# Optimization experiments

Hardware: AMD Instinct MI355X
Metric: run time of the kernel (lower is better)

The kernel has to match this reference:

```python
import jax, jax.numpy as jnp
import numpy as np
from math import sqrt

N_HEADS = 4
IN_FEATURES = 64
KQ = 64
HEAD_V = IN_FEATURES // N_HEADS  # 16


def setup_inputs() -> dict:
    key = jax.random.key(0)
    ks = jax.random.split(key, 7)
    s = 0.05
    x = jax.random.normal(ks[0], (8192, IN_FEATURES), dtype=jnp.float32)
    # Per-head Linear weights stacked on a leading head axis.
    # torch Linear: y = x @ W.T + b; we store W already transposed: [H, F, E]
    Wq = jax.random.normal(ks[1], (N_HEADS, IN_FEATURES, KQ), dtype=jnp.float32) * s
    bq = jax.random.normal(ks[2], (N_HEADS, KQ), dtype=jnp.float32) * s
    Wk = jax.random.normal(ks[3], (N_HEADS, IN_FEATURES, KQ), dtype=jnp.float32) * s
    bk = jax.random.normal(ks[4], (N_HEADS, KQ), dtype=jnp.float32) * s
    Wv = jax.random.normal(ks[5], (N_HEADS, IN_FEATURES, HEAD_V), dtype=jnp.float32) * s
    bv = jax.random.normal(ks[6], (N_HEADS, HEAD_V), dtype=jnp.float32) * s
    return {"x": x, "Wq": Wq, "bq": bq, "Wk": Wk, "bk": bk, "Wv": Wv, "bv": bv}


def reference(x, Wq, bq, Wk, bk, Wv, bv):
    N, F = x.shape
    scale = 1.0 / sqrt(F)  # original divides by sqrt(in_features), NOT sqrt(kq)
    # Batched-head projections: [H, N, E]
    Q = jnp.einsum('nf,hfe->hne', x, Wq) + bq[:, None, :]
    K = jnp.einsum('nf,hfe->hne', x, Wk) + bk[:, None, :]
    V = jnp.einsum('nf,hfd->hnd', x, Wv) + bv[:, None, :]
    logits = jnp.einsum('hne,hme->hnm', Q, K) * scale  # [H, N, N]
    attn = jax.nn.softmax(logits, axis=-1)
    out_heads = jnp.einsum('hnm,hmd->hnd', attn, V)    # [H, N, HEAD_V]
    # Head i writes columns [i*HEAD_V:(i+1)*HEAD_V] of the output.
    out = jnp.transpose(out_heads, (1, 0, 2)).reshape(N, F)
    return out
```

## Files before the change

### kernel.cpp

```cpp
#include <hip/hip_runtime.h>

typedef __attribute__((ext_vector_type(4))) float f32x4;
typedef __attribute__((ext_vector_type(8))) short bf16x8;
typedef __attribute__((ext_vector_type(4))) short bf16x4;
typedef long fp8x8;

#define NH 4

static __device__ __forceinline__ unsigned short f2bf(float f){
  unsigned u = __float_as_uint(f);
  u += 0x7FFFu + ((u >> 16) & 1u);
  return (unsigned short)(u >> 16);
}

static __device__ __forceinline__ unsigned pack2bf(float a, float b){
  return __builtin_amdgcn_perm(__float_as_uint(b) + 0x8000u,
                               __float_as_uint(a) + 0x8000u, 0x07060302u);
}

static __device__ __forceinline__ unsigned pack2bf_t(float a, float b){
  return __builtin_amdgcn_perm(__float_as_uint(b), __float_as_uint(a), 0x07060302u);
}

static __device__ __forceinline__ int pack_fp8x4(float a, float b, float c, float d){
  int w = __builtin_amdgcn_cvt_pk_fp8_f32(a, b, 0, false);
  w     = __builtin_amdgcn_cvt_pk_fp8_f32(c, d, w, true);
  return w;
}

__global__ __launch_bounds__(256) void wprep_kernel(
    const float* __restrict__ Wq, const float* __restrict__ bq,
    const float* __restrict__ Wk, const float* __restrict__ bk,
    const float* __restrict__ Wv,
    unsigned short* __restrict__ WF, float* __restrict__ bias_s, int n)
{
  __shared__ unsigned short wqT[64*72];
  __shared__ unsigned short wkT[64*72];
  __shared__ unsigned short wvT[16*72];

  const int t = threadIdx.x;
  const int h = blockIdx.x;
  const float S1 = 0.4246609001f;
  const int f = t >> 2, eg = t & 3;

  {
    const float4* g = (const float4*)(Wq + h*4096 + f*64 + eg*16);
    #pragma unroll
    for (int p = 0; p < 4; ++p){
      float4 d = g[p];
      int e0 = eg*16 + p*4;
      wqT[(e0+0)*72 + f] = f2bf(d.x * S1);
      wqT[(e0+1)*72 + f] = f2bf(d.y * S1);
      wqT[(e0+2)*72 + f] = f2bf(d.z * S1);
      wqT[(e0+3)*72 + f] = f2bf(d.w * S1);
    }
  }
  {
    const float4* g = (const float4*)(Wk + h*4096 + f*64 + eg*16);
    #pragma unroll
    for (int p = 0; p < 4; ++p){
      float4 d = g[p];
      int e0 = eg*16 + p*4;
      wkT[(e0+0)*72 + f] = f2bf(d.x * S1);
      wkT[(e0+1)*72 + f] = f2bf(d.y * S1);
      wkT[(e0+2)*72 + f] = f2bf(d.z * S1);
      wkT[(e0+3)*72 + f] = f2bf(d.w * S1);
    }
  }
  {
    float4 d = *(const float4*)(Wv + h*1024 + f*16 + eg*4);
    int d0 = eg*4;
    wvT[(d0+0)*72 + f] = f2bf(d.x);
    wvT[(d0+1)*72 + f] = f2bf(d.y);
    wvT[(d0+2)*72 + f] = f2bf(d.z);
    wvT[(d0+3)*72 + f] = f2bf(d.w);
  }
  if (t < 64)       bias_s[h*128 + t] = bq[h*64 + t] * S1;
  else if (t < 128) bias_s[h*128 + t] = bk[h*64 + (t-64)] * S1;
  __syncthreads();

  const int lane = t & 63, w = t >> 6;
  const int quad = lane >> 4, l16 = lane & 15;
  for (int s = w; s < 18; s += 4){
    const unsigned short* src;
    if (s < 8){      int et = s>>1,     ks = s&1;     src = wqT + (et*16+l16)*72 + ks*32 + quad*8; }
    else if (s < 16){int ft = (s-8)>>1, ks = (s-8)&1; src = wkT + (ft*16+l16)*72 + ks*32 + quad*8; }
    else {           int ks = s-16;                   src = wvT + l16*72 + ks*32 + quad*8; }
    uint4 v = *(const uint4*)src;
    *(uint4*)(WF + ((size_t)(h*18 + s)*64 + lane)*8) = v;
  }
}

__global__ __launch_bounds__(256) void proj_kernel(
    const float* __restrict__ x, const float* __restrict__ bv,
    const unsigned short* __restrict__ WF, const float* __restrict__ bias_s,
    unsigned char* __restrict__ Qfr, unsigned char* __restrict__ Kt,
    unsigned short* __restrict__ Vt, int n)
{
  __shared__ unsigned short xf[8*64*8];
  __shared__ float bql[64], bkl[64], bvl[16];

  const int t  = threadIdx.x;
  const int h  = blockIdx.y;
  const int r0 = blockIdx.x * 64;

  {
    const int r = t >> 2, cg4 = t & 3;
    const float4* g = (const float4*)(x + (size_t)(r0 + r)*64 + cg4*16);
    float4 a = g[0], b = g[1], c = g[2], d = g[3];
    unsigned u0 = pack2bf(a.x,a.y), u1 = pack2bf(a.z,a.w);
    unsigned u2 = pack2bf(b.x,b.y), u3 = pack2bf(b.z,b.w);
    unsigned u4 = pack2bf(c.x,c.y), u5 = pack2bf(c.z,c.w);
    unsigned u6 = pack2bf(d.x,d.y), u7 = pack2bf(d.z,d.w);
    const int it = r >> 4, l16r = r & 15, ks = cg4 >> 1, q0 = (cg4 & 1)*2;
    uint4* dst0 = (uint4*)(xf + ((it*2+ks)*64 + q0*16     + l16r)*8);
    uint4* dst1 = (uint4*)(xf + ((it*2+ks)*64 + (q0+1)*16 + l16r)*8);
    *dst0 = make_uint4(u0,u1,u2,u3);
    *dst1 = make_uint4(u4,u5,u6,u7);
  }
  if (t < 64)        bql[t]     = bias_s[h*128 + t];
  else if (t < 128)  bkl[t-64]  = bias_s[h*128 + t];
  else if (t < 144)  bvl[t-128] = bv[h*16 + (t-128)];
  __syncthreads();

  const int lane = t & 63, w = t >> 6;
  const int quad = lane >> 4, l16 = lane & 15;

  bf16x8 xa[8];
  #pragma unroll
  for (int i = 0; i < 8; ++i)
    xa[i] = *(const bf16x8*)(xf + (i*64 + lane)*8);

  const unsigned short* WFh = WF + (size_t)h*18*64*8;
  bf16x8 wq0 = *(const bf16x8*)(WFh + ((size_t)(     w*2 + 0)*64 + lane)*8);
  bf16x8 wq1 = *(const bf16x8*)(WFh + ((size_t)(     w*2 + 1)*64 + lane)*8);
  bf16x8 wk0 = *(const bf16x8*)(WFh + ((size_t)(8  + w*2 + 0)*64 + lane)*8);
  bf16x8 wk1 = *(const bf16x8*)(WFh + ((size_t)(8  + w*2 + 1)*64 + lane)*8);
  bf16x8 wv0 = *(const bf16x8*)(WFh + ((size_t)16*64 + lane)*8);
  bf16x8 wv1 = *(const bf16x8*)(WFh + ((size_t)17*64 + lane)*8);

  const f32x4 z = {0.f,0.f,0.f,0.f};
  f32x4 accQ[4] = {z,z,z,z};
  f32x4 accK[4] = {z,z,z,z};
  f32x4 accV = z;

  #pragma unroll
  for (int it = 0; it < 4; ++it){
    accQ[it] = __builtin_amdgcn_mfma_f32_16x16x32_bf16(wq0, xa[it*2+0], accQ[it], 0,0,0);
    accQ[it] = __builtin_amdgcn_mfma_f32_16x16x32_bf16(wq1, xa[it*2+1], accQ[it], 0,0,0);
  }
  #pragma unroll
  for (int tt = 0; tt < 4; ++tt){
    accK[tt] = __builtin_amdgcn_mfma_f32_16x16x32_bf16(wk0, xa[tt*2+0], accK[tt], 0,0,0);
    accK[tt] = __builtin_amdgcn_mfma_f32_16x16x32_bf16(wk1, xa[tt*2+1], accK[tt], 0,0,0);
  }
  accV = __builtin_amdgcn_mfma_f32_16x16x32_bf16(xa[w*2+0], wv0, accV, 0,0,0);
  accV = __builtin_amdgcn_mfma_f32_16x16x32_bf16(xa[w*2+1], wv1, accV, 0,0,0);

  {
    const int e0 = w*16 + quad*4;
    const float b0 = bql[e0], b1 = bql[e0+1], b2 = bql[e0+2], b3 = bql[e0+3];
    const int qk = (e0 & 31) >> 3, hf = e0 >> 5, boff = (quad & 1) * 4;
    #pragma unroll
    for (int it = 0; it < 4; ++it){
      unsigned o = pack_fp8x4(accQ[it][0]+b0, accQ[it][1]+b1,
                              accQ[it][2]+b2, accQ[it][3]+b3);
      const int T = (r0 >> 4) + it;
      *(unsigned*)(Qfr + (size_t)h*((size_t)n<<6) + (size_t)T*1024
                       + (qk*16 + l16)*16 + hf*8 + boff) = o;
    }
  }
  {
    const int f0 = w*16 + quad*4;
    const float bk0 = bkl[f0], bk1 = bkl[f0+1], bk2 = bkl[f0+2], bk3 = bkl[f0+3];
    const int qk = (f0 & 31) >> 3, hf = f0 >> 5, boff = (quad & 1) * 4;
    #pragma unroll
    for (int tt = 0; tt < 4; ++tt){
      unsigned o = pack_fp8x4(accK[tt][0]+bk0, accK[tt][1]+bk1,
                              accK[tt][2]+bk2, accK[tt][3]+bk3);
      const int T = (r0 >> 4) + tt;
      *(unsigned*)(Kt + (size_t)h*((size_t)n<<6) + (size_t)T*1024
                      + (qk*16 + l16)*16 + hf*8 + boff) = o;
    }
  }
  {
    float bvv = bvl[l16];
    unsigned v01 = pack2bf(accV[0]+bvv, accV[1]+bvv);
    unsigned v23 = pack2bf(accV[2]+bvv, accV[3]+bvv);
    const int T = (r0 >> 4) + w;
    *(uint2*)(Vt + (size_t)h*((size_t)n<<4)
                 + ((size_t)(T>>1)*64 + lane)*8 + (T&1)*4) = make_uint2(v01, v23);
  }
}

__global__ __launch_bounds__(512, 4) void attn_kernel(
    const unsigned char* __restrict__ Qfr, const unsigned char* __restrict__ Kt,
    const unsigned short* __restrict__ Vt, float* __restrict__ out, int n)
{
  __shared__ float part[7][64][33];

  const int tid  = threadIdx.x;
  const int lane = tid & 63;
  const int jq   = tid >> 6;

  #pragma unroll 1
  for (int i = 0; i < jq; ++i) __builtin_amdgcn_s_sleep(3);

  const int bid  = blockIdx.x;
  const int h    = bid & 3;
  const int iblk = bid >> 2;
  const int l16  = lane & 15, quad = lane >> 4;
  const int i0   = iblk*64;
  const int ntq  = (n >> 3) >> 4;
  const int nch  = ntq >> 1;
  const int tile0 = jq * ntq;

  const unsigned char* qfh = Qfr + (size_t)h*((size_t)n<<6);
  longlong2 q0 = *(const longlong2*)(qfh + (size_t)((i0>>4)    )*1024 + lane*16);
  longlong2 q1 = *(const longlong2*)(qfh + (size_t)((i0>>4) + 1)*1024 + lane*16);
  longlong2 q2 = *(const longlong2*)(qfh + (size_t)((i0>>4) + 2)*1024 + lane*16);
  longlong2 q3 = *(const longlong2*)(qfh + (size_t)((i0>>4) + 3)*1024 + lane*16);
  const fp8x8 qf00 = (fp8x8)q0.x, qf01 = (fp8x8)q0.y;
  const fp8x8 qf10 = (fp8x8)q1.x, qf11 = (fp8x8)q1.y;
  const fp8x8 qf20 = (fp8x8)q2.x, qf21 = (fp8x8)q2.y;
  const fp8x8 qf30 = (fp8x8)q3.x, qf31 = (fp8x8)q3.y;

  const longlong2* ktl = (const longlong2*)(Kt + (size_t)h*((size_t)n<<6)) + (size_t)tile0*64 + lane;
  const uint4*     vtu = (const uint4*)(Vt + (size_t)h*((size_t)n<<4)) + (size_t)(tile0>>1)*64 + lane;

  const f32x4 z = {0.f,0.f,0.f,0.f};
  f32x4 o0 = z, o1 = z, o2 = z, o3 = z;
  f32x4 la0 = z, la1 = z, la2 = z, la3 = z;
  const bf16x8 vones = {(short)0x3F80, (short)0x3F80, (short)0x3F80, (short)0x3F80,
                        (short)0x3F80, (short)0x3F80, (short)0x3F80, (short)0x3F80};

  longlong2 ka0 = ktl[0],   ka1 = ktl[64];
  uint4     va  = vtu[0];
  longlong2 kb0 = ktl[128], kb1 = ktl[192];
  uint4     vb  = vtu[64];

#define ITILE(QA, QB, OO, LL)                                                 \
  {                                                                           \
    f32x4 s = __builtin_amdgcn_mfma_f32_16x16x32_fp8_fp8(a0, QA, z, 0,0,0);   \
    s = __builtin_amdgcn_mfma_f32_16x16x32_fp8_fp8(a1, QB, s, 0,0,0);         \
    f32x4 u = __builtin_amdgcn_mfma_f32_16x16x32_fp8_fp8(b0, QA, z, 0,0,0);   \
    u = __builtin_amdgcn_mfma_f32_16x16x32_fp8_fp8(b1, QB, u, 0,0,0);         \
    float e0 = __builtin_amdgcn_exp2f(s[0]);                                  \
    float e1 = __builtin_amdgcn_exp2f(s[1]);                                  \
    float e2 = __builtin_amdgcn_exp2f(s[2]);                                  \
    float e3 = __builtin_amdgcn_exp2f(s[3]);                                  \
    float f0 = __builtin_amdgcn_exp2f(u[0]);                                  \
    float f1 = __builtin_amdgcn_exp2f(u[1]);                                  \
    float f2 = __builtin_amdgcn_exp2f(u[2]);                                  \
    float f3 = __builtin_amdgcn_exp2f(u[3]);                                  \
    union { uint4 uu; bf16x8 v; } pq;                                         \
    pq.uu = make_uint4(pack2bf_t(e0,e1), pack2bf_t(e2,e3),                    \
                       pack2bf_t(f0,f1), pack2bf_t(f2,f3));                   \
    OO = __builtin_amdgcn_mfma_f32_16x16x32_bf16(pq.v, vfv,   OO, 0,0,0);     \
    LL = __builtin_amdgcn_mfma_f32_16x16x32_bf16(pq.v, vones, LL, 0,0,0);     \
  }

#define ATTN_CHUNK(KA, KB, VV)                                                \
  {                                                                           \
    const fp8x8 a0 = (fp8x8)KA.x, a1 = (fp8x8)KA.y;                           \
    const fp8x8 b0 = (fp8x8)KB.x, b1 = (fp8x8)KB.y;                           \
    union { uint4 uu; bf16x8 v; } vfu; vfu.uu = VV;                           \
    const bf16x8 vfv = vfu.v;                                                 \
    ITILE(qf00, qf01, o0, la0)                                                \
    ITILE(qf10, qf11, o1, la1)                                                \
    ITILE(qf20, qf21, o2, la2)                                                \
    ITILE(qf30, qf31, o3, la3)                                                \
  }

  for (int c = 0; c < nch - 2; c += 2){
    ATTN_CHUNK(ka0, ka1, va)
    ka0 = ktl[256]; ka1 = ktl[320]; va = vtu[128];
    ATTN_CHUNK(kb0, kb1, vb)
    kb0 = ktl[384]; kb1 = ktl[448]; vb = vtu[192];
    ktl += 256; vtu += 128;
    #pragma unroll
    for (int g = 0; g < 12; ++g){
      __builtin_amdgcn_sched_group_barrier(0x008, 2, 0);
      __builtin_amdgcn_sched_group_barrier(0x002, 8, 0);
    }
  }
  ATTN_CHUNK(ka0, ka1, va)
  ATTN_CHUNK(kb0, kb1, vb)
#undef ATTN_CHUNK
#undef ITILE

  if (jq > 0){
    float* p = &part[jq-1][lane][0];
    p[ 0]=o0[0];  p[ 1]=o0[1];  p[ 2]=o0[2];  p[ 3]=o0[3];
    p[ 4]=o1[0];  p[ 5]=o1[1];  p[ 6]=o1[2];  p[ 7]=o1[3];
    p[ 8]=o2[0];  p[ 9]=o2[1];  p[10]=o2[2];  p[11]=o2[3];
    p[12]=o3[0];  p[13]=o3[1];  p[14]=o3[2];  p[15]=o3[3];
    p[16]=la0[0]; p[17]=la0[1]; p[18]=la0[2]; p[19]=la0[3];
    p[20]=la1[0]; p[21]=la1[1]; p[22]=la1[2]; p[23]=la1[3];
    p[24]=la2[0]; p[25]=la2[1]; p[26]=la2[2]; p[27]=la2[3];
    p[28]=la3[0]; p[29]=la3[1]; p[30]=la3[2]; p[31]=la3[3];
  }
  __syncthreads();

  if (jq == 0){
    #pragma unroll
    for (int q = 0; q < 7; ++q){
      const float* r = &part[q][lane][0];
      o0[0] +=r[0];  o0[1] +=r[1];  o0[2] +=r[2];  o0[3] +=r[3];
      o1[0] +=r[4];  o1[1] +=r[5];  o1[2] +=r[6];  o1[3] +=r[7];
      o2[0] +=r[8];  o2[1] +=r[9];  o2[2] +=r[10]; o2[3] +=r[11];
      o3[0] +=r[12]; o3[1] +=r[13]; o3[2] +=r[14]; o3[3] +=r[15];
      la0[0]+=r[16]; la0[1]+=r[17]; la0[2]+=r[18]; la0[3]+=r[19];
      la1[0]+=r[20]; la1[1]+=r[21]; la1[2]+=r[22]; la1[3]+=r[23];
      la2[0]+=r[24]; la2[1]+=r[25]; la2[2]+=r[26]; la2[3]+=r[27];
      la3[0]+=r[28]; la3[1]+=r[29]; la3[2]+=r[30]; la3[3]+=r[31];
    }
    #pragma unroll
    for (int reg = 0; reg < 4; ++reg){
      int i = quad*4 + reg;
      out[(size_t)(i0 +      i)*64 + h*16 + l16] = o0[reg] / la0[reg];
      out[(size_t)(i0 + 16 + i)*64 + h*16 + l16] = o1[reg] / la1[reg];
      out[(size_t)(i0 + 32 + i)*64 + h*16 + l16] = o2[reg] / la2[reg];
      out[(size_t)(i0 + 48 + i)*64 + h*16 + l16] = o3[reg] / la3[reg];
    }
  }
}

extern "C" void kernel_launch(void* const* d_in, const int* in_sizes, int n_in,
                              void* d_out, int out_size, void* d_ws, size_t ws_size,
                              hipStream_t stream) {
  const float* x  = (const float*)d_in[0];
  const float* Wq = (const float*)d_in[1];
  const float* bq = (const float*)d_in[2];
  const float* Wk = (const float*)d_in[3];
  const float* bk = (const float*)d_in[4];
  const float* Wv = (const float*)d_in[5];
  const float* bv = (const float*)d_in[6];
  float* out = (float*)d_out;

  const int n = in_sizes[0] / 64;

  unsigned char* Qfr  = (unsigned char*)d_ws;
  unsigned char* Kt   = Qfr + (size_t)NH*n*64;
  unsigned short* Vt  = (unsigned short*)(Kt + (size_t)NH*n*64);
  unsigned short* WF  = Vt + (size_t)NH*n*16;
  float* bias_s       = (float*)(WF + (size_t)NH*18*64*8);

  wprep_kernel<<<NH, 256, 0, stream>>>(Wq, bq, Wk, bk, Wv, WF, bias_s, n);
  proj_kernel<<<dim3(n/64, NH), 256, 0, stream>>>(x, bv, WF, bias_s, Qfr, Kt, Vt, n);
  attn_kernel<<<dim3((n/64)*NH), 512, 0, stream>>>(Qfr, Kt, Vt, out, n);
}
```

Measured before the change: 118.5 us.

## Fuse weight prep, projection and attention into one cooperative kernel

Merges the three launches (weight prep, QKV projection, attention) into a single cooperative kernel with a grid-wide sync between the projection and attention phases. Each block now redoes the weight transpose/convert in LDS (aliased onto the partial-sum buffer) instead of reading a prepared global copy. It also retunes the attention loop's scheduling group barriers. The three-kernel path is kept as a fallback if the cooperative launch fails. The aim is to remove launch gaps and tail effects, at the cost of a grid barrier, redundant per-block weight prep, and a requirement that all 512 blocks be co-resident.

```diff
diff --git a/kernel.cpp b/kernel.cpp
--- a/kernel.cpp
+++ b/kernel.cpp
@@ -1,8 +1,10 @@
 #include <hip/hip_runtime.h>
+#include <hip/hip_cooperative_groups.h>
+
+namespace cg = cooperative_groups;
 
 typedef __attribute__((ext_vector_type(4))) float f32x4;
 typedef __attribute__((ext_vector_type(8))) short bf16x8;
-typedef __attribute__((ext_vector_type(4))) short bf16x4;
 typedef long fp8x8;
 
 #define NH 4
@@ -27,217 +29,6 @@
   w     = __builtin_amdgcn_cvt_pk_fp8_f32(c, d, w, true);
   return w;
 }
-
-__global__ __launch_bounds__(256) void wprep_kernel(
-    const float* __restrict__ Wq, const float* __restrict__ bq,
-    const float* __restrict__ Wk, const float* __restrict__ bk,
-    const float* __restrict__ Wv,
-    unsigned short* __restrict__ WF, float* __restrict__ bias_s, int n)
-{
-  __shared__ unsigned short wqT[64*72];
-  __shared__ unsigned short wkT[64*72];
-  __shared__ unsigned short wvT[16*72];
-
-  const int t = threadIdx.x;
-  const int h = blockIdx.x;
-  const float S1 = 0.4246609001f;
-  const int f = t >> 2, eg = t & 3;
-
-  {
-    const float4* g = (const float4*)(Wq + h*4096 + f*64 + eg*16);
-    #pragma unroll
-    for (int p = 0; p < 4; ++p){
-      float4 d = g[p];
-      int e0 = eg*16 + p*4;
-      wqT[(e0+0)*72 + f] = f2bf(d.x * S1);
-      wqT[(e0+1)*72 + f] = f2bf(d.y * S1);
-      wqT[(e0+2)*72 + f] = f2bf(d.z * S1);
-      wqT[(e0+3)*72 + f] = f2bf(d.w * S1);
-    }
-  }
-  {
-    const float4* g = (const float4*)(Wk + h*4096 + f*64 + eg*16);
-    #pragma unroll
-    for (int p = 0; p < 4; ++p){
-      float4 d = g[p];
-      int e0 = eg*16 + p*4;
-      wkT[(e0+0)*72 + f] = f2bf(d.x * S1);
-      wkT[(e0+1)*72 + f] = f2bf(d.y * S1);
-      wkT[(e0+2)*72 + f] = f2bf(d.z * S1);
-      wkT[(e0+3)*72 + f] = f2bf(d.w * S1);
-    }
-  }
-  {
-    float4 d = *(const float4*)(Wv + h*1024 + f*16 + eg*4);
-    int d0 = eg*4;
-    wvT[(d0+0)*72 + f] = f2bf(d.x);
-    wvT[(d0+1)*72 + f] = f2bf(d.y);
-    wvT[(d0+2)*72 + f] = f2bf(d.z);
-    wvT[(d0+3)*72 + f] = f2bf(d.w);
-  }
-  if (t < 64)       bias_s[h*128 + t] = bq[h*64 + t] * S1;
-  else if (t < 128) bias_s[h*128 + t] = bk[h*64 + (t-64)] * S1;
-  __syncthreads();
-
-  const int lane = t & 63, w = t >> 6;
-  const int quad = lane >> 4, l16 = lane & 15;
-  for (int s = w; s < 18; s += 4){
-    const unsigned short* src;
-    if (s < 8){      int et = s>>1,     ks = s&1;     src = wqT + (et*16+l16)*72 + ks*32 + quad*8; }
-    else if (s < 16){int ft = (s-8)>>1, ks = (s-8)&1; src = wkT + (ft*16+l16)*72 + ks*32 + quad*8; }
-    else {           int ks = s-16;                   src = wvT + l16*72 + ks*32 + quad*8; }
-    uint4 v = *(const uint4*)src;
-    *(uint4*)(WF + ((size_t)(h*18 + s)*64 + lane)*8) = v;
-  }
-}
-
-__global__ __launch_bounds__(256) void proj_kernel(
-    const float* __restrict__ x, const float* __restrict__ bv,
-    const unsigned short* __restrict__ WF, const float* __restrict__ bias_s,
-    unsigned char* __restrict__ Qfr, unsigned char* __restrict__ Kt,
-    unsigned short* __restrict__ Vt, int n)
-{
-  __shared__ unsigned short xf[8*64*8];
-  __shared__ float bql[64], bkl[64], bvl[16];
-
-  const int t  = threadIdx.x;
-  const int h  = blockIdx.y;
-  const int r0 = blockIdx.x * 64;
-
-  {
-    const int r = t >> 2, cg4 = t & 3;
-    const float4* g = (const float4*)(x + (size_t)(r0 + r)*64 + cg4*16);
-    float4 a = g[0], b = g[1], c = g[2], d = g[3];
-    unsigned u0 = pack2bf(a.x,a.y), u1 = pack2bf(a.z,a.w);
-    unsigned u2 = pack2bf(b.x,b.y), u3 = pack2bf(b.z,b.w);
-    unsigned u4 = pack2bf(c.x,c.y), u5 = pack2bf(c.z,c.w);
-    unsigned u6 = pack2bf(d.x,d.y), u7 = pack2bf(d.z,d.w);
-    const int it = r >> 4, l16r = r & 15, ks = cg4 >> 1, q0 = (cg4 & 1)*2;
-    uint4* dst0 = (uint4*)(xf + ((it*2+ks)*64 + q0*16     + l16r)*8);
-    uint4* dst1 = (uint4*)(xf + ((it*2+ks)*64 + (q0+1)*16 + l16r)*8);
-    *dst0 = make_uint4(u0,u1,u2,u3);
-    *dst1 = make_uint4(u4,u5,u6,u7);
-  }
-  if (t < 64)        bql[t]     = bias_s[h*128 + t];
-  else if (t < 128)  bkl[t-64]  = bias_s[h*128 + t];
-  else if (t < 144)  bvl[t-128] = bv[h*16 + (t-128)];
-  __syncthreads();
-
-  const int lane = t & 63, w = t >> 6;
-  const int quad = lane >> 4, l16 = lane & 15;
-
-  bf16x8 xa[8];
-  #pragma unroll
-  for (int i = 0; i < 8; ++i)
-    xa[i] = *(const bf16x8*)(xf + (i*64 + lane)*8);
-
-  const unsigned short* WFh = WF + (size_t)h*18*64*8;
-  bf16x8 wq0 = *(const bf16x8*)(WFh + ((size_t)(     w*2 + 0)*64 + lane)*8);
-  bf16x8 wq1 = *(const bf16x8*)(WFh + ((size_t)(     w*2 + 1)*64 + lane)*8);
-  bf16x8 wk0 = *(const bf16x8*)(WFh + ((size_t)(8  + w*2 + 0)*64 + lane)*8);
-  bf16x8 wk1 = *(const bf16x8*)(WFh + ((size_t)(8  + w*2 + 1)*64 + lane)*8);
-  bf16x8 wv0 = *(const bf16x8*)(WFh + ((size_t)16*64 + lane)*8);
-  bf16x8 wv1 = *(const bf16x8*)(WFh + ((size_t)17*64 + lane)*8);
-
-  const f32x4 z = {0.f,0.f,0.f,0.f};
-  f32x4 accQ[4] = {z,z,z,z};
-  f32x4 accK[4] = {z,z,z,z};
-  f32x4 accV = z;
-
-  #pragma unroll
-  for (int it = 0; it < 4; ++it){
-    accQ[it] = __builtin_amdgcn_mfma_f32_16x16x32_bf16(wq0, xa[it*2+0], accQ[it], 0,0,0);
-    accQ[it] = __builtin_amdgcn_mfma_f32_16x16x32_bf16(wq1, xa[it*2+1], accQ[it], 0,0,0);
-  }
-  #pragma unroll
-  for (int tt = 0; tt < 4; ++tt){
-    accK[tt] = __builtin_amdgcn_mfma_f32_16x16x32_bf16(wk0, xa[tt*2+0], accK[tt], 0,0,0);
-    accK[tt] = __builtin_amdgcn_mfma_f32_16x16x32_bf16(wk1, xa[tt*2+1], accK[tt], 0,0,0);
-  }
-  accV = __builtin_amdgcn_mfma_f32_16x16x32_bf16(xa[w*2+0], wv0, accV, 0,0,0);
-  accV = __builtin_amdgcn_mfma_f32_16x16x32_bf16(xa[w*2+1], wv1, accV, 0,0,0);
-
-  {
-    const int e0 = w*16 + quad*4;
-    const float b0 = bql[e0], b1 = bql[e0+1], b2 = bql[e0+2], b3 = bql[e0+3];
-    const int qk = (e0 & 31) >> 3, hf = e0 >> 5, boff = (quad & 1) * 4;
-    #pragma unroll
-    for (int it = 0; it < 4; ++it){
-      unsigned o = pack_fp8x4(accQ[it][0]+b0, accQ[it][1]+b1,
-                              accQ[it][2]+b2, accQ[it][3]+b3);
-      const int T = (r0 >> 4) + it;
-      *(unsigned*)(Qfr + (size_t)h*((size_t)n<<6) + (size_t)T*1024
-                       + (qk*16 + l16)*16 + hf*8 + boff) = o;
-    }
-  }
-  {
-    const int f0 = w*16 + quad*4;
-    const float bk0 = bkl[f0], bk1 = bkl[f0+1], bk2 = bkl[f0+2], bk3 = bkl[f0+3];
-    const int qk = (f0 & 31) >> 3, hf = f0 >> 5, boff = (quad & 1) * 4;
-    #pragma unroll
-    for (int tt = 0; tt < 4; ++tt){
-      unsigned o = pack_fp8x4(accK[tt][0]+bk0, accK[tt][1]+bk1,
-                              accK[tt][2]+bk2, accK[tt][3]+bk3);
-      const int T = (r0 >> 4) + tt;
-      *(unsigned*)(Kt + (size_t)h*((size_t)n<<6) + (size_t)T*1024
-                      + (qk*16 + l16)*16 + hf*8 + boff) = o;
-    }
-  }
-  {
-    float bvv = bvl[l16];
-    unsigned v01 = pack2bf(accV[0]+bvv, accV[1]+bvv);
-    unsigned v23 = pack2bf(accV[2]+bvv, accV[3]+bvv);
-    const int T = (r0 >> 4) + w;
-    *(uint2*)(Vt + (size_t)h*((size_t)n<<4)
-                 + ((size_t)(T>>1)*64 + lane)*8 + (T&1)*4) = make_uint2(v01, v23);
-  }
-}
-
-__global__ __launch_bounds__(512, 4) void attn_kernel(
-    const unsigned char* __restrict__ Qfr, const unsigned char* __restrict__ Kt,
-    const unsigned short* __restrict__ Vt, float* __restrict__ out, int n)
-{
-  __shared__ float part[7][64][33];
-
-  const int tid  = threadIdx.x;
-  const int lane = tid & 63;
-  const int jq   = tid >> 6;
-
-  #pragma unroll 1
-  for (int i = 0; i < jq; ++i) __builtin_amdgcn_s_sleep(3);
-
-  const int bid  = blockIdx.x;
-  const int h    = bid & 3;
-  const int iblk = bid >> 2;
-  const int l16  = lane & 15, quad = lane >> 4;
-  const int i0   = iblk*64;
-  const int ntq  = (n >> 3) >> 4;
-  const int nch  = ntq >> 1;
-  const int tile0 = jq * ntq;
-
-  const unsigned char* qfh = Qfr + (size_t)h*((size_t)n<<6);
-  longlong2 q0 = *(const longlong2*)(qfh + (size_t)((i0>>4)    )*1024 + lane*16);
-  longlong2 q1 = *(const longlong2*)(qfh + (size_t)((i0>>4) + 1)*1024 + lane*16);
-  longlong2 q2 = *(const longlong2*)(qfh + (size_t)((i0>>4) + 2)*1024 + lane*16);
-  longlong2 q3 = *(const longlong2*)(qfh + (size_t)((i0>>4) + 3)*1024 + lane*16);
-  const fp8x8 qf00 = (fp8x8)q0.x, qf01 = (fp8x8)q0.y;
-  const fp8x8 qf10 = (fp8x8)q1.x, qf11 = (fp8x8)q1.y;
-  const fp8x8 qf20 = (fp8x8)q2.x, qf21 = (fp8x8)q2.y;
-  const fp8x8 qf30 = (fp8x8)q3.x, qf31 = (fp8x8)q3.y;
-
-  const longlong2* ktl = (const longlong2*)(Kt + (size_t)h*((size_t)n<<6)) + (size_t)tile0*64 + lane;
-  const uint4*     vtu = (const uint4*)(Vt + (size_t)h*((size_t)n<<4)) + (size_t)(tile0>>1)*64 + lane;
-
-  const f32x4 z = {0.f,0.f,0.f,0.f};
-  f32x4 o0 = z, o1 = z, o2 = z, o3 = z;
-  f32x4 la0 = z, la1 = z, la2 = z, la3 = z;
-  const bf16x8 vones = {(short)0x3F80, (short)0x3F80, (short)0x3F80, (short)0x3F80,
-                        (short)0x3F80, (short)0x3F80, (short)0x3F80, (short)0x3F80};
-
-  longlong2 ka0 = ktl[0],   ka1 = ktl[64];
-  uint4     va  = vtu[0];
-  longlong2 kb0 = ktl[128], kb1 = ktl[192];
-  uint4     vb  = vtu[64];
 
 #define ITILE(QA, QB, OO, LL)                                                 \
   {                                                                           \
@@ -272,22 +63,468 @@
     ITILE(qf30, qf31, o3, la3)                                                \
   }
 
+#define ATTN_SGB                                                              \
+    _Pragma("unroll")                                                         \
+    for (int g = 0; g < 16; ++g){                                             \
+      __builtin_amdgcn_sched_group_barrier(0x008, 3, 0);                      \
+      __builtin_amdgcn_sched_group_barrier(0x002, 6, 0);                      \
+    }
+
+__global__ __launch_bounds__(512, 4) void fused_kernel(
+    const float* __restrict__ x,
+    const float* __restrict__ Wq, const float* __restrict__ bq,
+    const float* __restrict__ Wk, const float* __restrict__ bk,
+    const float* __restrict__ Wv, const float* __restrict__ bv,
+    unsigned char* __restrict__ Qfr, unsigned char* __restrict__ Kt,
+    unsigned short* __restrict__ Vt, float* __restrict__ out, int n)
+{
+  __shared__ float part[7][64][33];
+  __shared__ float bql[64], bkl[64], bvl[16];
+
+  unsigned short* wqT = (unsigned short*)&part[0][0][0];
+  unsigned short* wkT = wqT + 64*72;
+  unsigned short* wvT = wkT + 64*72;
+  unsigned short* xf  = (unsigned short*)&part[0][0][0];
+
+  const int t    = threadIdx.x;
+  const int lane = t & 63;
+  const int w    = t >> 6;
+  const int bid  = blockIdx.x;
+  const int h    = bid & 3;
+  const int iblk = bid >> 2;
+  const int r0   = iblk * 64;
+  const int quad = lane >> 4, l16 = lane & 15;
+  const float S1 = 0.4246609001f;
+  const f32x4 z  = {0.f,0.f,0.f,0.f};
+
+  if (t < 256){
+    const int f = t >> 2, eg = t & 3;
+    {
+      const float4* g = (const float4*)(Wq + h*4096 + f*64 + eg*16);
+      #pragma unroll
+      for (int p = 0; p < 4; ++p){
+        float4 d = g[p]; int e0 = eg*16 + p*4;
+        wqT[(e0+0)*72 + f] = f2bf(d.x * S1);
+        wqT[(e0+1)*72 + f] = f2bf(d.y * S1);
+        wqT[(e0+2)*72 + f] = f2bf(d.z * S1);
+        wqT[(e0+3)*72 + f] = f2bf(d.w * S1);
+      }
+    }
+    {
+      const float4* g = (const float4*)(Wk + h*4096 + f*64 + eg*16);
+      #pragma unroll
+      for (int p = 0; p < 4; ++p){
+        float4 d = g[p]; int e0 = eg*16 + p*4;
+        wkT[(e0+0)*72 + f] = f2bf(d.x * S1);
+        wkT[(e0+1)*72 + f] = f2bf(d.y * S1);
+        wkT[(e0+2)*72 + f] = f2bf(d.z * S1);
+        wkT[(e0+3)*72 + f] = f2bf(d.w * S1);
+      }
+    }
+    {
+      float4 d = *(const float4*)(Wv + h*1024 + f*16 + eg*4);
+      int d0 = eg*4;
+      wvT[(d0+0)*72 + f] = f2bf(d.x);
+      wvT[(d0+1)*72 + f] = f2bf(d.y);
+      wvT[(d0+2)*72 + f] = f2bf(d.z);
+      wvT[(d0+3)*72 + f] = f2bf(d.w);
+    }
+  }
+  if (t < 64)        bql[t]     = bq[h*64 + t] * S1;
+  else if (t < 128)  bkl[t-64]  = bk[h*64 + (t-64)] * S1;
+  else if (t < 144)  bvl[t-128] = bv[h*16 + (t-128)];
+  __syncthreads();
+
+  bf16x8 wq0 = {0,0,0,0,0,0,0,0}, wq1 = wq0, wk0 = wq0, wk1 = wq0,
+         wv0 = wq0, wv1 = wq0;
+  if (w < 4){
+    wq0 = *(const bf16x8*)(wqT + (w*16 + l16)*72 +      quad*8);
+    wq1 = *(const bf16x8*)(wqT + (w*16 + l16)*72 + 32 + quad*8);
+    wk0 = *(const bf16x8*)(wkT + (w*16 + l16)*72 +      quad*8);
+    wk1 = *(const bf16x8*)(wkT + (w*16 + l16)*72 + 32 + quad*8);
+    wv0 = *(const bf16x8*)(wvT + l16*72 +      quad*8);
+    wv1 = *(const bf16x8*)(wvT + l16*72 + 32 + quad*8);
+  }
+  __syncthreads();
+
+  if (t < 256){
+    const int r = t >> 2, cg4 = t & 3;
+    const float4* g = (const float4*)(x + (size_t)(r0 + r)*64 + cg4*16);
+    float4 a = g[0], b = g[1], c = g[2], d = g[3];
+    unsigned u0 = pack2bf(a.x,a.y), u1 = pack2bf(a.z,a.w);
+    unsigned u2 = pack2bf(b.x,b.y), u3 = pack2bf(b.z,b.w);
+    unsigned u4 = pack2bf(c.x,c.y), u5 = pack2bf(c.z,c.w);
+    unsigned u6 = pack2bf(d.x,d.y), u7 = pack2bf(d.z,d.w);
+    const int it = r >> 4, l16r = r & 15, ks = cg4 >> 1, q0 = (cg4 & 1)*2;
+    uint4* dst0 = (uint4*)(xf + ((it*2+ks)*64 + q0*16     + l16r)*8);
+    uint4* dst1 = (uint4*)(xf + ((it*2+ks)*64 + (q0+1)*16 + l16r)*8);
+    *dst0 = make_uint4(u0,u1,u2,u3);
+    *dst1 = make_uint4(u4,u5,u6,u7);
+  }
+  __syncthreads();
+
+  if (w < 4){
+    bf16x8 xa[8];
+    #pragma unroll
+    for (int i = 0; i < 8; ++i)
+      xa[i] = *(const bf16x8*)(xf + (i*64 + lane)*8);
+
+    f32x4 accQ[4] = {z,z,z,z};
+    f32x4 accK[4] = {z,z,z,z};
+    f32x4 accV = z;
+
+    #pragma unroll
+    for (int it = 0; it < 4; ++it){
+      accQ[it] = __builtin_amdgcn_mfma_f32_16x16x32_bf16(wq0, xa[it*2+0], accQ[it], 0,0,0);
+      accQ[it] = __builtin_amdgcn_mfma_f32_16x16x32_bf16(wq1, xa[it*2+1], accQ[it], 0,0,0);
+    }
+    #pragma unroll
+    for (int tt = 0; tt < 4; ++tt){
+      accK[tt] = __builtin_amdgcn_mfma_f32_16x16x32_bf16(wk0, xa[tt*2+0], accK[tt], 0,0,0);
+      accK[tt] = __builtin_amdgcn_mfma_f32_16x16x32_bf16(wk1, xa[tt*2+1], accK[tt], 0,0,0);
+    }
+    accV = __builtin_amdgcn_mfma_f32_16x16x32_bf16(xa[w*2+0], wv0, accV, 0,0,0);
+    accV = __builtin_amdgcn_mfma_f32_16x16x32_bf16(xa[w*2+1], wv1, accV, 0,0,0);
+
+    {
+      const int e0 = w*16 + quad*4;
+      const float b0 = bql[e0], b1 = bql[e0+1], b2 = bql[e0+2], b3 = bql[e0+3];
+      const int qk = (e0 & 31) >> 3, hf = e0 >> 5, boff = (quad & 1) * 4;
+      #pragma unroll
+      for (int it = 0; it < 4; ++it){
+        unsigned o = pack_fp8x4(accQ[it][0]+b0, accQ[it][1]+b1,
+                                accQ[it][2]+b2, accQ[it][3]+b3);
+        const int T = (r0 >> 4) + it;
+        *(unsigned*)(Qfr + (size_t)h*((size_t)n<<6) + (size_t)T*1024
+                         + (qk*16 + l16)*16 + hf*8 + boff) = o;
+      }
+    }
+    {
+      const int f0 = w*16 + quad*4;
+      const float bk0 = bkl[f0], bk1 = bkl[f0+1], bk2 = bkl[f0+2], bk3 = bkl[f0+3];
+      const int qk = (f0 & 31) >> 3, hf = f0 >> 5, boff = (quad & 1) * 4;
+      #pragma unroll
+      for (int tt = 0; tt < 4; ++tt){
+        unsigned o = pack_fp8x4(accK[tt][0]+bk0, accK[tt][1]+bk1,
+                                accK[tt][2]+bk2, accK[tt][3]+bk3);
+        const int T = (r0 >> 4) + tt;
+        *(unsigned*)(Kt + (size_t)h*((size_t)n<<6) + (size_t)T*1024
+                        + (qk*16 + l16)*16 + hf*8 + boff) = o;
+      }
+    }
+    {
+      float bvv = bvl[l16];
+      unsigned v01 = pack2bf(accV[0]+bvv, accV[1]+bvv);
+      unsigned v23 = pack2bf(accV[2]+bvv, accV[3]+bvv);
+      const int T = (r0 >> 4) + w;
+      *(uint2*)(Vt + (size_t)h*((size_t)n<<4)
+                   + ((size_t)(T>>1)*64 + lane)*8 + (T&1)*4) = make_uint2(v01, v23);
+    }
+  }
+
+  __threadfence();
+  cg::this_grid().sync();
+
+  const int jq = w;
+
+  #pragma unroll 1
+  for (int i = 0; i < jq; ++i) __builtin_amdgcn_s_sleep(3);
+
+  const int i0  = r0;
+  const int ntq = (n >> 3) >> 4;
+  const int nch = ntq >> 1;
+  const int tile0 = jq * ntq;
+
+  const unsigned char* qfh = Qfr + (size_t)h*((size_t)n<<6);
+  longlong2 q0 = *(const longlong2*)(qfh + (size_t)((i0>>4)    )*1024 + lane*16);
+  longlong2 q1 = *(const longlong2*)(qfh + (size_t)((i0>>4) + 1)*1024 + lane*16);
+  longlong2 q2 = *(const longlong2*)(qfh + (size_t)((i0>>4) + 2)*1024 + lane*16);
+  longlong2 q3 = *(const longlong2*)(qfh + (size_t)((i0>>4) + 3)*1024 + lane*16);
+  const fp8x8 qf00 = (fp8x8)q0.x, qf01 = (fp8x8)q0.y;
+  const fp8x8 qf10 = (fp8x8)q1.x, qf11 = (fp8x8)q1.y;
+  const fp8x8 qf20 = (fp8x8)q2.x, qf21 = (fp8x8)q2.y;
+  const fp8x8 qf30 = (fp8x8)q3.x, qf31 = (fp8x8)q3.y;
+
+  const longlong2* ktl = (const longlong2*)(Kt + (size_t)h*((size_t)n<<6)) + (size_t)tile0*64 + lane;
+  const uint4*     vtu = (const uint4*)(Vt + (size_t)h*((size_t)n<<4)) + (size_t)(tile0>>1)*64 + lane;
+
+  f32x4 o0 = z, o1 = z, o2 = z, o3 = z;
+  f32x4 la0 = z, la1 = z, la2 = z, la3 = z;
+  const bf16x8 vones = {(short)0x3F80, (short)0x3F80, (short)0x3F80, (short)0x3F80,
+                        (short)0x3F80, (short)0x3F80, (short)0x3F80, (short)0x3F80};
+
+  longlong2 ka0 = ktl[0],   ka1 = ktl[64];
+  uint4     va  = vtu[0];
+  longlong2 kb0 = ktl[128], kb1 = ktl[192];
+  uint4     vb  = vtu[64];
+
   for (int c = 0; c < nch - 2; c += 2){
     ATTN_CHUNK(ka0, ka1, va)
     ka0 = ktl[256]; ka1 = ktl[320]; va = vtu[128];
     ATTN_CHUNK(kb0, kb1, vb)
     kb0 = ktl[384]; kb1 = ktl[448]; vb = vtu[192];
     ktl += 256; vtu += 128;
-    #pragma unroll
-    for (int g = 0; g < 12; ++g){
-      __builtin_amdgcn_sched_group_barrier(0x008, 2, 0);
-      __builtin_amdgcn_sched_group_barrier(0x002, 8, 0);
-    }
+    ATTN_SGB
   }
   ATTN_CHUNK(ka0, ka1, va)
   ATTN_CHUNK(kb0, kb1, vb)
-#undef ATTN_CHUNK
-#undef ITILE
+
+  if (jq > 0){
+    float* p = &part[jq-1][lane][0];
+    p[ 0]=o0[0];  p[ 1]=o0[1];  p[ 2]=o0[2];  p[ 3]=o0[3];
+    p[ 4]=o1[0];  p[ 5]=o1[1];  p[ 6]=o1[2];  p[ 7]=o1[3];
+    p[ 8]=o2[0];  p[ 9]=o2[1];  p[10]=o2[2];  p[11]=o2[3];
+    p[12]=o3[0];  p[13]=o3[1];  p[14]=o3[2];  p[15]=o3[3];
+    p[16]=la0[0]; p[17]=la0[1]; p[18]=la0[2]; p[19]=la0[3];
+    p[20]=la1[0]; p[21]=la1[1]; p[22]=la1[2]; p[23]=la1[3];
+    p[24]=la2[0]; p[25]=la2[1]; p[26]=la2[2]; p[27]=la2[3];
+    p[28]=la3[0]; p[29]=la3[1]; p[30]=la3[2]; p[31]=la3[3];
+  }
+  __syncthreads();
+
+  if (jq == 0){
+    #pragma unroll
+    for (int q = 0; q < 7; ++q){
+      const float* r = &part[q][lane][0];
+      o0[0] +=r[0];  o0[1] +=r[1];  o0[2] +=r[2];  o0[3] +=r[3];
+      o1[0] +=r[4];  o1[1] +=r[5];  o1[2] +=r[6];  o1[3] +=r[7];
+      o2[0] +=r[8];  o2[1] +=r[9];  o2[2] +=r[10]; o2[3] +=r[11];
+      o3[0] +=r[12]; o3[1] +=r[13]; o3[2] +=r[14]; o3[3] +=r[15];
+      la0[0]+=r[16]; la0[1]+=r[17]; la0[2]+=r[18]; la0[3]+=r[19];
+      la1[0]+=r[20]; la1[1]+=r[21]; la1[2]+=r[22]; la1[3]+=r[23];
+      la2[0]+=r[24]; la2[1]+=r[25]; la2[2]+=r[26]; la2[3]+=r[27];
+      la3[0]+=r[28]; la3[1]+=r[29]; la3[2]+=r[30]; la3[3]+=r[31];
+    }
+    #pragma unroll
+    for (int reg = 0; reg < 4; ++reg){
+      int i = quad*4 + reg;
+      out[(size_t)(i0 +      i)*64 + h*16 + l16] = o0[reg] / la0[reg];
+      out[(size_t)(i0 + 16 + i)*64 + h*16 + l16] = o1[reg] / la1[reg];
+      out[(size_t)(i0 + 32 + i)*64 + h*16 + l16] = o2[reg] / la2[reg];
+      out[(size_t)(i0 + 48 + i)*64 + h*16 + l16] = o3[reg] / la3[reg];
+    }
+  }
+}
+
+__global__ __launch_bounds__(256) void wprep_kernel(
+    const float* __restrict__ Wq, const float* __restrict__ bq,
+    const float* __restrict__ Wk, const float* __restrict__ bk,
+    const float* __restrict__ Wv,
+    unsigned short* __restrict__ WF, float* __restrict__ bias_s, int n)
+{
+  __shared__ unsigned short wqT[64*72];
+  __shared__ unsigned short wkT[64*72];
+  __shared__ unsigned short wvT[16*72];
+
+  const int t = threadIdx.x;
+  const int h = blockIdx.x;
+  const float S1 = 0.4246609001f;
+  const int f = t >> 2, eg = t & 3;
+
+  {
+    const float4* g = (const float4*)(Wq + h*4096 + f*64 + eg*16);
+    #pragma unroll
+    for (int p = 0; p < 4; ++p){
+      float4 d = g[p]; int e0 = eg*16 + p*4;
+      wqT[(e0+0)*72 + f] = f2bf(d.x * S1);
+      wqT[(e0+1)*72 + f] = f2bf(d.y * S1);
+      wqT[(e0+2)*72 + f] = f2bf(d.z * S1);
+      wqT[(e0+3)*72 + f] = f2bf(d.w * S1);
+    }
+  }
+  {
+    const float4* g = (const float4*)(Wk + h*4096 + f*64 + eg*16);
+    #pragma unroll
+    for (int p = 0; p < 4; ++p){
+      float4 d = g[p]; int e0 = eg*16 + p*4;
+      wkT[(e0+0)*72 + f] = f2bf(d.x * S1);
+      wkT[(e0+1)*72 + f] = f2bf(d.y * S1);
+      wkT[(e0+2)*72 + f] = f2bf(d.z * S1);
+      wkT[(e0+3)*72 + f] = f2bf(d.w * S1);
+    }
+  }
+  {
+    float4 d = *(const float4*)(Wv + h*1024 + f*16 + eg*4);
+    int d0 = eg*4;
+    wvT[(d0+0)*72 + f] = f2bf(d.x);
+    wvT[(d0+1)*72 + f] = f2bf(d.y);
+    wvT[(d0+2)*72 + f] = f2bf(d.z);
+    wvT[(d0+3)*72 + f] = f2bf(d.w);
+  }
+  if (t < 64)       bias_s[h*128 + t] = bq[h*64 + t] * S1;
+  else if (t < 128) bias_s[h*128 + t] = bk[h*64 + (t-64)] * S1;
+  __syncthreads();
+
+  const int lane = t & 63, w = t >> 6;
+  const int quad = lane >> 4, l16 = lane & 15;
+  for (int s = w; s < 18; s += 4){
+    const unsigned short* src;
+    if (s < 8){      int et = s>>1,     ks = s&1;     src = wqT + (et*16+l16)*72 + ks*32 + quad*8; }
+    else if (s < 16){int ft = (s-8)>>1, ks = (s-8)&1; src = wkT + (ft*16+l16)*72 + ks*32 + quad*8; }
+    else {           int ks = s-16;                   src = wvT + l16*72 + ks*32 + quad*8; }
+    uint4 v = *(const uint4*)src;
+    *(uint4*)(WF + ((size_t)(h*18 + s)*64 + lane)*8) = v;
+  }
+}
+
+__global__ __launch_bounds__(256) void proj_kernel(
+    const float* __restrict__ x, const float* __restrict__ bv,
+    const unsigned short* __restrict__ WF, const float* __restrict__ bias_s,
+    unsigned char* __restrict__ Qfr, unsigned char* __restrict__ Kt,
+    unsigned short* __restrict__ Vt, int n)
+{
+  __shared__ unsigned short xf[8*64*8];
+  __shared__ float bql[64], bkl[64], bvl[16];
+
+  const int t  = threadIdx.x;
+  const int h  = blockIdx.y;
+  const int r0 = blockIdx.x * 64;
+
+  {
+    const int r = t >> 2, cg4 = t & 3;
+    const float4* g = (const float4*)(x + (size_t)(r0 + r)*64 + cg4*16);
+    float4 a = g[0], b = g[1], c = g[2], d = g[3];
+    unsigned u0 = pack2bf(a.x,a.y), u1 = pack2bf(a.z,a.w);
+    unsigned u2 = pack2bf(b.x,b.y), u3 = pack2bf(b.z,b.w);
+    unsigned u4 = pack2bf(c.x,c.y), u5 = pack2bf(c.z,c.w);
+    unsigned u6 = pack2bf(d.x,d.y), u7 = pack2bf(d.z,d.w);
+    const int it = r >> 4, l16r = r & 15, ks = cg4 >> 1, q0 = (cg4 & 1)*2;
+    uint4* dst0 = (uint4*)(xf + ((it*2+ks)*64 + q0*16     + l16r)*8);
+    uint4* dst1 = (uint4*)(xf + ((it*2+ks)*64 + (q0+1)*16 + l16r)*8);
+    *dst0 = make_uint4(u0,u1,u2,u3);
+    *dst1 = make_uint4(u4,u5,u6,u7);
+  }
+  if (t < 64)        bql[t]     = bias_s[h*128 + t];
+  else if (t < 128)  bkl[t-64]  = bias_s[h*128 + t];
+  else if (t < 144)  bvl[t-128] = bv[h*16 + (t-128)];
+  __syncthreads();
+
+  const int lane = t & 63, w = t >> 6;
+  const int quad = lane >> 4, l16 = lane & 15;
+
+  bf16x8 xa[8];
+  #pragma unroll
+  for (int i = 0; i < 8; ++i)
+    xa[i] = *(const bf16x8*)(xf + (i*64 + lane)*8);
+
+  const unsigned short* WFh = WF + (size_t)h*18*64*8;
+  bf16x8 wq0 = *(const bf16x8*)(WFh + ((size_t)(     w*2 + 0)*64 + lane)*8);
+  bf16x8 wq1 = *(const bf16x8*)(WFh + ((size_t)(     w*2 + 1)*64 + lane)*8);
+  bf16x8 wk0 = *(const bf16x8*)(WFh + ((size_t)(8  + w*2 + 0)*64 + lane)*8);
+  bf16x8 wk1 = *(const bf16x8*)(WFh + ((size_t)(8  + w*2 + 1)*64 + lane)*8);
+  bf16x8 wv0 = *(const bf16x8*)(WFh + ((size_t)16*64 + lane)*8);
+  bf16x8 wv1 = *(const bf16x8*)(WFh + ((size_t)17*64 + lane)*8);
+
+  const f32x4 z = {0.f,0.f,0.f,0.f};
+  f32x4 accQ[4] = {z,z,z,z};
+  f32x4 accK[4] = {z,z,z,z};
+  f32x4 accV = z;
+
+  #pragma unroll
+  for (int it = 0; it < 4; ++it){
+    accQ[it] = __builtin_amdgcn_mfma_f32_16x16x32_bf16(wq0, xa[it*2+0], accQ[it], 0,0,0);
+    accQ[it] = __builtin_amdgcn_mfma_f32_16x16x32_bf16(wq1, xa[it*2+1], accQ[it], 0,0,0);
+  }
+  #pragma unroll
+  for (int tt = 0; tt < 4; ++tt){
+    accK[tt] = __builtin_amdgcn_mfma_f32_16x16x32_bf16(wk0, xa[tt*2+0], accK[tt], 0,0,0);
+    accK[tt] = __builtin_amdgcn_mfma_f32_16x16x32_bf16(wk1, xa[tt*2+1], accK[tt], 0,0,0);
+  }
+  accV = __builtin_amdgcn_mfma_f32_16x16x32_bf16(xa[w*2+0], wv0, accV, 0,0,0);
+  accV = __builtin_amdgcn_mfma_f32_16x16x32_bf16(xa[w*2+1], wv1, accV, 0,0,0);
+
+  {
+    const int e0 = w*16 + quad*4;
+    const float b0 = bql[e0], b1 = bql[e0+1], b2 = bql[e0+2], b3 = bql[e0+3];
+    const int qk = (e0 & 31) >> 3, hf = e0 >> 5, boff = (quad & 1) * 4;
+    #pragma unroll
+    for (int it = 0; it < 4; ++it){
+      unsigned o = pack_fp8x4(accQ[it][0]+b0, accQ[it][1]+b1,
+                              accQ[it][2]+b2, accQ[it][3]+b3);
+      const int T = (r0 >> 4) + it;
+      *(unsigned*)(Qfr + (size_t)h*((size_t)n<<6) + (size_t)T*1024
+                       + (qk*16 + l16)*16 + hf*8 + boff) = o;
+    }
+  }
+  {
+    const int f0 = w*16 + quad*4;
+    const float bk0 = bkl[f0], bk1 = bkl[f0+1], bk2 = bkl[f0+2], bk3 = bkl[f0+3];
+    const int qk = (f0 & 31) >> 3, hf = f0 >> 5, boff = (quad & 1) * 4;
+    #pragma unroll
+    for (int tt = 0; tt < 4; ++tt){
+      unsigned o = pack_fp8x4(accK[tt][0]+bk0, accK[tt][1]+bk1,
+                              accK[tt][2]+bk2, accK[tt][3]+bk3);
+      const int T = (r0 >> 4) + tt;
+      *(unsigned*)(Kt + (size_t)h*((size_t)n<<6) + (size_t)T*1024
+                      + (qk*16 + l16)*16 + hf*8 + boff) = o;
+    }
+  }
+  {
+    float bvv = bvl[l16];
+    unsigned v01 = pack2bf(accV[0]+bvv, accV[1]+bvv);
+    unsigned v23 = pack2bf(accV[2]+bvv, accV[3]+bvv);
+    const int T = (r0 >> 4) + w;
+    *(uint2*)(Vt + (size_t)h*((size_t)n<<4)
+                 + ((size_t)(T>>1)*64 + lane)*8 + (T&1)*4) = make_uint2(v01, v23);
+  }
+}
+
+__global__ __launch_bounds__(512, 4) void attn_kernel(
+    const unsigned char* __restrict__ Qfr, const unsigned char* __restrict__ Kt,
+    const unsigned short* __restrict__ Vt, float* __restrict__ out, int n)
+{
+  __shared__ float part[7][64][33];
+
+  const int tid  = threadIdx.x;
+  const int lane = tid & 63;
+  const int jq   = tid >> 6;
+
+  #pragma unroll 1
+  for (int i = 0; i < jq; ++i) __builtin_amdgcn_s_sleep(3);
+
+  const int bid  = blockIdx.x;
+  const int h    = bid & 3;
+  const int iblk = bid >> 2;
+  const int l16  = lane & 15, quad = lane >> 4;
+  const int i0   = iblk*64;
+  const int ntq  = (n >> 3) >> 4;
+  const int nch  = ntq >> 1;
+  const int tile0 = jq * ntq;
+
+  const unsigned char* qfh = Qfr + (size_t)h*((size_t)n<<6);
+  longlong2 q0 = *(const longlong2*)(qfh + (size_t)((i0>>4)    )*1024 + lane*16);
+  longlong2 q1 = *(const longlong2*)(qfh + (size_t)((i0>>4) + 1)*1024 + lane*16);
+  longlong2 q2 = *(const longlong2*)(qfh + (size_t)((i0>>4) + 2)*1024 + lane*16);
+  longlong2 q3 = *(const longlong2*)(qfh + (size_t)((i0>>4) + 3)*1024 + lane*16);
+  const fp8x8 qf00 = (fp8x8)q0.x, qf01 = (fp8x8)q0.y;
+  const fp8x8 qf10 = (fp8x8)q1.x, qf11 = (fp8x8)q1.y;
+  const fp8x8 qf20 = (fp8x8)q2.x, qf21 = (fp8x8)q2.y;
+  const fp8x8 qf30 = (fp8x8)q3.x, qf31 = (fp8x8)q3.y;
+
+  const longlong2* ktl = (const longlong2*)(Kt + (size_t)h*((size_t)n<<6)) + (size_t)tile0*64 + lane;
+  const uint4*     vtu = (const uint4*)(Vt + (size_t)h*((size_t)n<<4)) + (size_t)(tile0>>1)*64 + lane;
+
+  const f32x4 z = {0.f,0.f,0.f,0.f};
+  f32x4 o0 = z, o1 = z, o2 = z, o3 = z;
+  f32x4 la0 = z, la1 = z, la2 = z, la3 = z;
+  const bf16x8 vones = {(short)0x3F80, (short)0x3F80, (short)0x3F80, (short)0x3F80,
+                        (short)0x3F80, (short)0x3F80, (short)0x3F80, (short)0x3F80};
+
+  longlong2 ka0 = ktl[0],   ka1 = ktl[64];
+  uint4     va  = vtu[0];
+  longlong2 kb0 = ktl[128], kb1 = ktl[192];
+  uint4     vb  = vtu[64];
+
+  for (int c = 0; c < nch - 2; c += 2){
+    ATTN_CHUNK(ka0, ka1, va)
+    ka0 = ktl[256]; ka1 = ktl[320]; va = vtu[128];
+    ATTN_CHUNK(kb0, kb1, vb)
+    kb0 = ktl[384]; kb1 = ktl[448]; vb = vtu[192];
+    ktl += 256; vtu += 128;
+    ATTN_SGB
+  }
+  ATTN_CHUNK(ka0, ka1, va)
+  ATTN_CHUNK(kb0, kb1, vb)
 
   if (jq > 0){
     float* p = &part[jq-1][lane][0];
@@ -338,7 +575,7 @@
   const float* bv = (const float*)d_in[6];
   float* out = (float*)d_out;
 
-  const int n = in_sizes[0] / 64;
+  int n = in_sizes[0] / 64;
 
   unsigned char* Qfr  = (unsigned char*)d_ws;
   unsigned char* Kt   = Qfr + (size_t)NH*n*64;
@@ -346,7 +583,18 @@
   unsigned short* WF  = Vt + (size_t)NH*n*16;
   float* bias_s       = (float*)(WF + (size_t)NH*18*64*8);
 
-  wprep_kernel<<<NH, 256, 0, stream>>>(Wq, bq, Wk, bk, Wv, WF, bias_s, n);
-  proj_kernel<<<dim3(n/64, NH), 256, 0, stream>>>(x, bv, WF, bias_s, Qfr, Kt, Vt, n);
-  attn_kernel<<<dim3((n/64)*NH), 512, 0, stream>>>(Qfr, Kt, Vt, out, n);
-}
+  void* params[12];
+  params[0]  = (void*)&x;   params[1]  = (void*)&Wq;  params[2]  = (void*)&bq;
+  params[3]  = (void*)&Wk;  params[4]  = (void*)&bk;  params[5]  = (void*)&Wv;
+  params[6]  = (void*)&bv;  params[7]  = (void*)&Qfr; params[8]  = (void*)&Kt;
+  params[9]  = (void*)&Vt;  params[10] = (void*)&out; params[11] = (void*)&n;
+
+  hipError_t err = hipLaunchCooperativeKernel(
+      (const void*)fused_kernel, dim3((n/64)*NH), dim3(512), params, 0u, stream);
+
+  if (err != hipSuccess){
+    wprep_kernel<<<NH, 256, 0, stream>>>(Wq, bq, Wk, bk, Wv, WF, bias_s, n);
+    proj_kernel<<<dim3(n/64, NH), 256, 0, stream>>>(x, bv, WF, bias_s, Qfr, Kt, Vt, n);
+    attn_kernel<<<dim3((n/64)*NH), 512, 0, stream>>>(Qfr, Kt, Vt, out, n);
+  }
+}
```

New measurement: 253.3 us. 2.14x slower.
